# Performance work log

Hardware: AMD Instinct MI355X
Metric: run time of the kernel (lower is better)

Reference implementation:

```python
import jax, jax.numpy as jnp
import numpy as np

N, C_IN, C_OUT, NS, SP = 100000, 64, 64, 16, 8
MID = C_OUT
EPS = 1e-5


def _bn(t, g, b):
    # BatchNorm1d training-mode stats over (n, k) per channel (biased var, as torch)
    m = t.mean(axis=(0, 1))
    v = t.var(axis=(0, 1))
    return g * (t - m) / jnp.sqrt(v + EPS) + b


def setup_inputs() -> dict:
    key = jax.random.key(0)
    ks = jax.random.split(key, 24)
    s = 0.05
    d = {
        'p': jax.random.normal(ks[0], (N, 3), jnp.float32),
        'x': jax.random.normal(ks[1], (N, C_IN), jnp.float32),
        'knn_idx': jax.random.randint(ks[2], (N, NS), 0, N, jnp.int64),
        # channelMixMLPs01: Linear(3+in, ns) + Bilinear(ns, ns, ns)
        'w1': jax.random.normal(ks[3], (NS, 3 + C_IN), jnp.float32) * s,
        'b1': jnp.zeros((NS,), jnp.float32),
        'bw': jax.random.normal(ks[4], (NS, NS, NS), jnp.float32) * s,
        'bb': jnp.zeros((NS,), jnp.float32),
        # linear_p: Linear(3,3) -> BN(3) -> ReLU -> Linear(3,out)
        'lp_w1': jax.random.normal(ks[5], (3, 3), jnp.float32) * s,
        'lp_b1': jnp.zeros((3,), jnp.float32),
        'bnp_g': jnp.ones((3,), jnp.float32),
        'bnp_b': jnp.zeros((3,), jnp.float32),
        'lp_w2': jax.random.normal(ks[6], (C_OUT, 3), jnp.float32) * s,
        'lp_b2': jnp.zeros((C_OUT,), jnp.float32),
        'c1_w': jax.random.normal(ks[7], (MID, 2 * NS), jnp.float32) * s,
        'bn1_g': jnp.ones((MID,), jnp.float32),
        'bn1_b': jnp.zeros((MID,), jnp.float32),
        'c2_w': jax.random.normal(ks[8], (MID // SP, MID), jnp.float32) * s,
        'bn2_g': jnp.ones((MID // SP,), jnp.float32),
        'bn2_b': jnp.zeros((MID // SP,), jnp.float32),
        'c3_w': jax.random.normal(ks[9], (C_OUT // SP, MID // SP), jnp.float32) * s,
        'c3_b': jnp.zeros((C_OUT // SP,), jnp.float32),
        # channelMixMLPs03: Linear(in, out)
        'w3': jax.random.normal(ks[10], (C_OUT, C_IN), jnp.float32) * s,
        'b3': jnp.zeros((C_OUT,), jnp.float32),
    }
    return d


def reference(p, x, knn_idx, w1, b1, bw, bb, lp_w1, lp_b1, bnp_g, bnp_b,
              lp_w2, lp_b2, c1_w, bn1_g, bn1_b, c2_w, bn2_g, bn2_b,
              c3_w, c3_b, w3, b3):
    n = p.shape[0]
    # queryandgroup (use_xyz=True): gather neighbors, relative coords + feats
    p_r = p[knn_idx] - p[:, None, :]                 # [n, k, 3]
    x_knn = jnp.concatenate([p_r, x[knn_idx]], -1)   # [n, k, 3+c_in]
    # channelMixMLPs01: Linear -> ReLU -> Bilinear(e, e)
    e = jax.nn.relu(x_knn @ w1.T + b1)               # [n, k, ns]
    e = jnp.einsum('nki,oij,nkj->nko', e, bw, e) + bb
    # linear_p on relative coords
    pe = p_r @ lp_w1.T + lp_b1                       # [n, k, 3]
    pe = jax.nn.relu(_bn(pe, bnp_g, bnp_b))
    p_embed = pe @ lp_w2.T + lp_b2                   # [n, k, out]
    # shrink_p: n k (a b) -> sum over a -> [n, k, ns]
    p_shrink = p_embed.reshape(n, NS, C_OUT // NS, NS).sum(axis=2)
    energy = jnp.concatenate([e, p_shrink], -1)
    # channelMixMLPs02 (1x1 convs == per-point linears over channel dim)
    h = jax.nn.relu(_bn(energy @ c1_w.T, bn1_g, bn1_b))
    h = jax.nn.relu(_bn(h @ c2_w.T, bn2_g, bn2_b))
    w = jax.nn.softmax(h @ c3_w.T + c3_b, axis=1)    # [n, k, out/sp]
    # value path: Linear then gather by knn_idx
    x_v = (x @ w3.T + b3)[knn_idx]                   # [n, k, out]
    xk = (x_v + p_embed).reshape(n, NS, SP, C_OUT // SP)
    xk = (xk * w[:, :, None, :]).reshape(n, NS, C_OUT)
    x_out = xk.sum(axis=1)                           # [n, out]
    return (x_out, xk, knn_idx, p_r)
```

## Files before the change

kernel.cpp:

```cpp
#include <hip/hip_runtime.h>
#include <math.h>

#define NPTS 100000
#define KNB  16
#define NK   1600000

#define OUT_XK   6400000
#define OUT_KNN  108800000
#define OUT_PR   110400000

#define WS_BNP_RAW 0
#define WS_BN1_RAW 6
#define WS_BN2_RAW 134
#define WS_BNP_SS  160
#define WS_WS2     166
#define WS_WSB     214
#define WS_BN1_SS  230
#define WS_BN2_SS  358
#define WS_SYM     384
#define WS_C1F     2560
#define WS_C2T     2816
#define WS_E       4096
#define WS_T2      25604096
#define WS_XROW    38404096
#define WS_X1      44804096

#define GRID_NK 3125
#define NK_STRIDE 800000


__global__ __launch_bounds__(256) void k_pre(
    const float* __restrict__ x, const float* __restrict__ w3,
    const float* __restrict__ b3, const float* __restrict__ w1,
    const float* __restrict__ b1, float* __restrict__ ws)
{
    int n = blockIdx.x * 256 + threadIdx.x;
    if (n >= NPTS) return;
    float xr[64];
    const float4* xp = (const float4*)(x + (size_t)n * 64);
    #pragma unroll
    for (int i = 0; i < 16; ++i) {
        float4 v = xp[i];
        xr[4*i] = v.x; xr[4*i+1] = v.y; xr[4*i+2] = v.z; xr[4*i+3] = v.w;
    }
    float* xrow = ws + WS_XROW;
    for (int c = 0; c < 64; ++c) {
        const float* wr = w3 + c * 64;
        float a0 = b3[c], a1 = 0.f;
        #pragma unroll
        for (int q = 0; q < 64; q += 2) { a0 += wr[q] * xr[q]; a1 += wr[q+1] * xr[q+1]; }
        xrow[(size_t)n * 64 + c] = a0 + a1;
    }
    float* X1 = ws + WS_X1;
    for (int j = 0; j < 16; ++j) {
        const float* wr = w1 + j * 67 + 3;
        float a0 = b1[j], a1 = 0.f;
        #pragma unroll
        for (int q = 0; q < 64; q += 2) { a0 += wr[q] * xr[q]; a1 += wr[q+1] * xr[q+1]; }
        X1[n * 16 + j] = a0 + a1;
    }
}

__global__ void k_sym(const float* __restrict__ bw, float* __restrict__ ws)
{
    int t = blockIdx.x * 256 + threadIdx.x;
    if (t >= 136 * 16) return;
    int pair = t >> 4, o = t & 15;
    int i = 0, r = pair;
    while (r >= 16 - i) { r -= 16 - i; ++i; }
    int j = i + r;
    float v = bw[o * 256 + i * 16 + j];
    if (i != j) v += bw[o * 256 + j * 16 + i];
    ws[WS_SYM + pair * 16 + o] = v;
}

__global__ __launch_bounds__(256) void k_stage0(
    const float* __restrict__ p, const int* __restrict__ knn,
    const float* __restrict__ w1, const float* __restrict__ bb,
    const float* __restrict__ lpw1, const float* __restrict__ lpb1,
    const float* __restrict__ wsro, float* __restrict__ ws, float* __restrict__ out)
{
    __shared__ float wsym[136 * 16];
    __shared__ float e1s[2][16][256];
    __shared__ float sb[6];
    const float* symw = wsro + WS_SYM;
    const float* X1   = wsro + WS_X1;
    float* e_out = ws + WS_E;
    float* o_knn = out + OUT_KNN;
    float* o_pr  = out + OUT_PR;
    int tid = threadIdx.x;
    if (tid < 6) sb[tid] = 0.f;
    for (int k = tid; k < 136 * 16; k += 256) wsym[k] = symw[k];

    int gid = blockIdx.x * 256 + tid;
    int id0 = gid * 2;
    int n = id0 >> 4;
    float px = p[n*3+0], py = p[n*3+1], pz = p[n*3+2];
    float ps0=0.f, ps1=0.f, ps2=0.f, pq0=0.f, pq1=0.f, pq2=0.f;

    #pragma unroll
    for (int e = 0; e < 2; ++e) {
        int id = id0 + e;
        int idx = knn[id];
        float pr0 = p[idx*3+0] - px;
        float pr1 = p[idx*3+1] - py;
        float pr2 = p[idx*3+2] - pz;
        o_pr[id*3+0] = pr0; o_pr[id*3+1] = pr1; o_pr[id*3+2] = pr2;
        o_knn[id] = (float)idx;
        float v0 = lpb1[0] + lpw1[0]*pr0 + lpw1[1]*pr1 + lpw1[2]*pr2;
        float v1 = lpb1[1] + lpw1[3]*pr0 + lpw1[4]*pr1 + lpw1[5]*pr2;
        float v2 = lpb1[2] + lpw1[6]*pr0 + lpw1[7]*pr1 + lpw1[8]*pr2;
        ps0 += v0; ps1 += v1; ps2 += v2;
        pq0 += v0*v0; pq1 += v1*v1; pq2 += v2*v2;
        const float4* xg = (const float4*)(X1 + (size_t)idx * 16);
        #pragma unroll
        for (int h = 0; h < 4; ++h) {
            float4 v = xg[h];
            const float* wr = w1 + (4*h) * 67;
            e1s[e][4*h+0][tid] = fmaxf(v.x + wr[0]*pr0 + wr[1]*pr1 + wr[2]*pr2, 0.f);
            wr += 67;
            e1s[e][4*h+1][tid] = fmaxf(v.y + wr[0]*pr0 + wr[1]*pr1 + wr[2]*pr2, 0.f);
            wr += 67;
            e1s[e][4*h+2][tid] = fmaxf(v.z + wr[0]*pr0 + wr[1]*pr1 + wr[2]*pr2, 0.f);
            wr += 67;
            e1s[e][4*h+3][tid] = fmaxf(v.w + wr[0]*pr0 + wr[1]*pr1 + wr[2]*pr2, 0.f);
        }
    }
    __syncthreads();

    float acc_a[16], acc_b[16];
    #pragma unroll
    for (int o = 0; o < 16; ++o) { float bo = bb[o]; acc_a[o] = bo; acc_b[o] = bo; }

    int pair = 0;
    #pragma unroll 1
    for (int i = 0; i < 16; ++i) {
        float eai = e1s[0][i][tid];
        float ebi = e1s[1][i][tid];
        #pragma unroll 1
        for (int j = i; j < 16; ++j, ++pair) {
            float eaj = e1s[0][j][tid];
            float ebj = e1s[1][j][tid];
            float ma = eai * eaj, mb = ebi * ebj;
            const float4* wp = (const float4*)(wsym + pair * 16);
            float4 w0v = wp[0], w1v = wp[1], w2v = wp[2], w3v = wp[3];
            acc_a[0]  += w0v.x*ma; acc_a[1]  += w0v.y*ma; acc_a[2]  += w0v.z*ma; acc_a[3]  += w0v.w*ma;
            acc_a[4]  += w1v.x*ma; acc_a[5]  += w1v.y*ma; acc_a[6]  += w1v.z*ma; acc_a[7]  += w1v.w*ma;
            acc_a[8]  += w2v.x*ma; acc_a[9]  += w2v.y*ma; acc_a[10] += w2v.z*ma; acc_a[11] += w2v.w*ma;
            acc_a[12] += w3v.x*ma; acc_a[13] += w3v.y*ma; acc_a[14] += w3v.z*ma; acc_a[15] += w3v.w*ma;
            acc_b[0]  += w0v.x*mb; acc_b[1]  += w0v.y*mb; acc_b[2]  += w0v.z*mb; acc_b[3]  += w0v.w*mb;
            acc_b[4]  += w1v.x*mb; acc_b[5]  += w1v.y*mb; acc_b[6]  += w1v.z*mb; acc_b[7]  += w1v.w*mb;
            acc_b[8]  += w2v.x*mb; acc_b[9]  += w2v.y*mb; acc_b[10] += w2v.z*mb; acc_b[11] += w2v.w*mb;
            acc_b[12] += w3v.x*mb; acc_b[13] += w3v.y*mb; acc_b[14] += w3v.z*mb; acc_b[15] += w3v.w*mb;
        }
    }
    float4* eo = (float4*)(e_out + (size_t)id0 * 16);
    eo[0] = make_float4(acc_a[0],  acc_a[1],  acc_a[2],  acc_a[3]);
    eo[1] = make_float4(acc_a[4],  acc_a[5],  acc_a[6],  acc_a[7]);
    eo[2] = make_float4(acc_a[8],  acc_a[9],  acc_a[10], acc_a[11]);
    eo[3] = make_float4(acc_a[12], acc_a[13], acc_a[14], acc_a[15]);
    eo[4] = make_float4(acc_b[0],  acc_b[1],  acc_b[2],  acc_b[3]);
    eo[5] = make_float4(acc_b[4],  acc_b[5],  acc_b[6],  acc_b[7]);
    eo[6] = make_float4(acc_b[8],  acc_b[9],  acc_b[10], acc_b[11]);
    eo[7] = make_float4(acc_b[12], acc_b[13], acc_b[14], acc_b[15]);

    #pragma unroll
    for (int off = 32; off; off >>= 1) {
        ps0 += __shfl_xor(ps0, off); ps1 += __shfl_xor(ps1, off); ps2 += __shfl_xor(ps2, off);
        pq0 += __shfl_xor(pq0, off); pq1 += __shfl_xor(pq1, off); pq2 += __shfl_xor(pq2, off);
    }
    if ((tid & 63) == 0) {
        atomicAdd(&sb[0], ps0); atomicAdd(&sb[1], ps1); atomicAdd(&sb[2], ps2);
        atomicAdd(&sb[3], pq0); atomicAdd(&sb[4], pq1); atomicAdd(&sb[5], pq2);
    }
    __syncthreads();
    if (tid < 6) atomicAdd(&ws[WS_BNP_RAW + tid], sb[tid]);
}

__global__ void k_fin_bnp(float* __restrict__ ws,
    const float* __restrict__ g, const float* __restrict__ b,
    const float* __restrict__ lpw2, const float* __restrict__ lpb2)
{
    int t = threadIdx.x;
    if (t < 3) {
        float mean = ws[WS_BNP_RAW + t] / (float)NK;
        float var  = ws[WS_BNP_RAW + 3 + t] / (float)NK - mean * mean;
        float sc = g[t] * rsqrtf(var + 1e-5f);
        ws[WS_BNP_SS + t] = sc;
        ws[WS_BNP_SS + 3 + t] = b[t] - mean * sc;
    }
    if (t >= 16 && t < 64) {
        int r = t - 16, j = r / 3, d = r % 3;
        ws[WS_WS2 + r] = lpw2[(j)*3+d] + lpw2[(16+j)*3+d] + lpw2[(32+j)*3+d] + lpw2[(48+j)*3+d];
    }
    if (t >= 64 && t < 80) {
        int j = t - 64;
        ws[WS_WSB + j] = lpb2[j] + lpb2[16+j] + lpb2[32+j] + lpb2[48+j];
    }
}

__global__ void k_fold(const float* __restrict__ c1w, const float* __restrict__ c2w,
                       float* __restrict__ ws)
{
    int c = threadIdx.x;
    if (c >= 64) return;
    const float* B = c1w + c * 32 + 16;
    float m0 = 0.f, m1 = 0.f, m2 = 0.f, dd = 0.f;
    #pragma unroll
    for (int j = 0; j < 16; ++j) {
        float bj = B[j];
        m0 += bj * ws[WS_WS2 + j*3 + 0];
        m1 += bj * ws[WS_WS2 + j*3 + 1];
        m2 += bj * ws[WS_WS2 + j*3 + 2];
        dd += bj * ws[WS_WSB + j];
    }
    ws[WS_C1F + c*4 + 0] = m0;
    ws[WS_C1F + c*4 + 1] = m1;
    ws[WS_C1F + c*4 + 2] = m2;
    ws[WS_C1F + c*4 + 3] = dd;
    #pragma unroll
    for (int k = 0; k < 8; ++k)
        ws[WS_C2T + c*8 + k] = c2w[k * 64 + c];
}

__device__ __forceinline__ void build_eq(
    const float* __restrict__ e_in, const float* __restrict__ o_pr,
    const float* __restrict__ lpw1, const float* __restrict__ lpb1,
    const float* __restrict__ wsro, int id, float* e, float* q)
{
    const float4* ep = (const float4*)(e_in + (size_t)id * 16);
    #pragma unroll
    for (int i = 0; i < 4; ++i) {
        float4 v = ep[i];
        e[4*i] = v.x; e[4*i+1] = v.y; e[4*i+2] = v.z; e[4*i+3] = v.w;
    }
    float pr0 = o_pr[id*3+0], pr1 = o_pr[id*3+1], pr2 = o_pr[id*3+2];
    float v0 = lpb1[0] + lpw1[0]*pr0 + lpw1[1]*pr1 + lpw1[2]*pr2;
    float v1 = lpb1[1] + lpw1[3]*pr0 + lpw1[4]*pr1 + lpw1[5]*pr2;
    float v2 = lpb1[2] + lpw1[6]*pr0 + lpw1[7]*pr1 + lpw1[8]*pr2;
    q[0] = fmaxf(v0*wsro[WS_BNP_SS+0] + wsro[WS_BNP_SS+3], 0.f);
    q[1] = fmaxf(v1*wsro[WS_BNP_SS+1] + wsro[WS_BNP_SS+4], 0.f);
    q[2] = fmaxf(v2*wsro[WS_BNP_SS+2] + wsro[WS_BNP_SS+5], 0.f);
}

__global__ __launch_bounds__(256) void k_stats1(
    const float* __restrict__ wsro, const float* __restrict__ out_ro,
    const float* __restrict__ lpw1, const float* __restrict__ lpb1,
    const float* __restrict__ c1w, float* __restrict__ ws)
{
    __shared__ float sacc[128];
    if (threadIdx.x < 128) sacc[threadIdx.x] = 0.f;
    __syncthreads();
    const float* e_in = wsro + WS_E;
    const float* o_pr = out_ro + OUT_PR;
    int id0 = blockIdx.x * 256 + threadIdx.x;
    int id1 = id0 + NK_STRIDE;
    float e0[16], e1[16], q0[3], q1[3];
    build_eq(e_in, o_pr, lpw1, lpb1, wsro, id0, e0, q0);
    build_eq(e_in, o_pr, lpw1, lpb1, wsro, id1, e1, q1);
    #pragma unroll 1
    for (int c = 0; c < 64; c += 2) {
        const float* wa = c1w + c * 32;
        const float* wb = wa + 32;
        const float4 fa = *(const float4*)(wsro + WS_C1F + c*4);
        const float4 fb = *(const float4*)(wsro + WS_C1F + c*4 + 4);
        float hA0 = fa.w + fa.x*q0[0] + fa.y*q0[1] + fa.z*q0[2];
        float hB0 = fb.w + fb.x*q0[0] + fb.y*q0[1] + fb.z*q0[2];
        float hA1 = fa.w + fa.x*q1[0] + fa.y*q1[1] + fa.z*q1[2];
        float hB1 = fb.w + fb.x*q1[0] + fb.y*q1[1] + fb.z*q1[2];
        #pragma unroll
        for (int k = 0; k < 16; ++k) {
            hA0 += wa[k]*e0[k]; hB0 += wb[k]*e0[k];
            hA1 += wa[k]*e1[k]; hB1 += wb[k]*e1[k];
        }
        float sA = hA0 + hA1, qA = hA0*hA0 + hA1*hA1;
        float sB = hB0 + hB1, qB = hB0*hB0 + hB1*hB1;
        #pragma unroll
        for (int off = 32; off; off >>= 1) {
            sA += __shfl_xor(sA, off); qA += __shfl_xor(qA, off);
            sB += __shfl_xor(sB, off); qB += __shfl_xor(qB, off);
        }
        if ((threadIdx.x & 63) == 0) {
            atomicAdd(&sacc[c], sA);   atomicAdd(&sacc[64+c], qA);
            atomicAdd(&sacc[c+1], sB); atomicAdd(&sacc[65+c], qB);
        }
    }
    __syncthreads();
    if (threadIdx.x < 128) atomicAdd(&ws[WS_BN1_RAW + threadIdx.x], sacc[threadIdx.x]);
}

__global__ void k_fin_bn1(float* __restrict__ ws, const float* __restrict__ g, const float* __restrict__ b)
{
    int c = threadIdx.x;
    if (c < 64) {
        float mean = ws[WS_BN1_RAW + c] / (float)NK;
        float var  = ws[WS_BN1_RAW + 64 + c] / (float)NK - mean * mean;
        float sc = g[c] * rsqrtf(var + 1e-5f);
        ws[WS_BN1_SS + c] = sc;
        ws[WS_BN1_SS + 64 + c] = b[c] - mean * sc;
    }
}

__global__ __launch_bounds__(256) void k_stage2(
    const float* __restrict__ wsro, const float* __restrict__ out_ro,
    const float* __restrict__ lpw1, const float* __restrict__ lpb1,
    const float* __restrict__ c1w, float* __restrict__ ws)
{
    float tsum[8] = {0,0,0,0,0,0,0,0}, tssq[8] = {0,0,0,0,0,0,0,0};
    const float* e_in = wsro + WS_E;
    const float* o_pr = out_ro + OUT_PR;
    float* t2 = ws + WS_T2;
    int id = blockIdx.x * 256 + threadIdx.x;
    #pragma unroll 1
    for (int it = 0; it < 2; ++it, id += NK_STRIDE) {
        float e[16], q[3];
        build_eq(e_in, o_pr, lpw1, lpb1, wsro, id, e, q);
        float t2a[8] = {0,0,0,0,0,0,0,0};
        #pragma unroll 1
        for (int c = 0; c < 64; c += 2) {
            const float* wa = c1w + c * 32;
            const float* wb = wa + 32;
            const float4 fa = *(const float4*)(wsro + WS_C1F + c*4);
            const float4 fb = *(const float4*)(wsro + WS_C1F + c*4 + 4);
            float h0 = fa.w + fa.x*q[0] + fa.y*q[1] + fa.z*q[2];
            float h1 = fb.w + fb.x*q[0] + fb.y*q[1] + fb.z*q[2];
            #pragma unroll
            for (int k = 0; k < 16; ++k) {
                h0 += wa[k]*e[k]; h1 += wb[k]*e[k];
            }
            h0 = fmaxf(h0 * wsro[WS_BN1_SS + c]     + wsro[WS_BN1_SS + 64 + c], 0.f);
            h1 = fmaxf(h1 * wsro[WS_BN1_SS + c + 1] + wsro[WS_BN1_SS + 65 + c], 0.f);
            const float4 ca0 = *(const float4*)(wsro + WS_C2T + c*8);
            const float4 ca1 = *(const float4*)(wsro + WS_C2T + c*8 + 4);
            const float4 cb0 = *(const float4*)(wsro + WS_C2T + c*8 + 8);
            const float4 cb1 = *(const float4*)(wsro + WS_C2T + c*8 + 12);
            t2a[0] += h0*ca0.x + h1*cb0.x; t2a[1] += h0*ca0.y + h1*cb0.y;
            t2a[2] += h0*ca0.z + h1*cb0.z; t2a[3] += h0*ca0.w + h1*cb0.w;
            t2a[4] += h0*ca1.x + h1*cb1.x; t2a[5] += h0*ca1.y + h1*cb1.y;
            t2a[6] += h0*ca1.z + h1*cb1.z; t2a[7] += h0*ca1.w + h1*cb1.w;
        }
        float4* t2p = (float4*)(t2 + (size_t)id * 8);
        t2p[0] = make_float4(t2a[0], t2a[1], t2a[2], t2a[3]);
        t2p[1] = make_float4(t2a[4], t2a[5], t2a[6], t2a[7]);
        #pragma unroll
        for (int c2 = 0; c2 < 8; ++c2) { tsum[c2] += t2a[c2]; tssq[c2] += t2a[c2] * t2a[c2]; }
    }
    __shared__ float sacc[16];
    if (threadIdx.x < 16) sacc[threadIdx.x] = 0.f;
    __syncthreads();
    #pragma unroll
    for (int c2 = 0; c2 < 8; ++c2) {
        float s = tsum[c2], s2 = tssq[c2];
        #pragma unroll
        for (int off = 32; off; off >>= 1) { s += __shfl_xor(s, off); s2 += __shfl_xor(s2, off); }
        if ((threadIdx.x & 63) == 0) { atomicAdd(&sacc[c2], s); atomicAdd(&sacc[8 + c2], s2); }
    }
    __syncthreads();
    if (threadIdx.x < 16) atomicAdd(&ws[WS_BN2_RAW + threadIdx.x], sacc[threadIdx.x]);
}

__global__ void k_fin_bn2(float* __restrict__ ws, const float* __restrict__ g, const float* __restrict__ b)
{
    int c = threadIdx.x;
    if (c < 8) {
        float mean = ws[WS_BN2_RAW + c] / (float)NK;
        float var  = ws[WS_BN2_RAW + 8 + c] / (float)NK - mean * mean;
        float sc = g[c] * rsqrtf(var + 1e-5f);
        ws[WS_BN2_SS + c] = sc;
        ws[WS_BN2_SS + 8 + c] = b[c] - mean * sc;
    }
}

__global__ __launch_bounds__(128) void k_final(
    const int* __restrict__ knn, const float* __restrict__ wsro,
    const float* __restrict__ c3w, const float* __restrict__ c3b,
    const float* __restrict__ lpw1, const float* __restrict__ lpb1,
    const float* __restrict__ lpw2, const float* __restrict__ lpb2,
    float* __restrict__ out)
{
    int n = blockIdx.x, t = threadIdx.x;
    __shared__ float h2s[16][8], ssm[16][8], wls[16][8], pes[16][3], prs[48], red[128];
    __shared__ int idxs[16];
    const float* t2   = wsro + WS_T2;
    const float* o_pr = out + OUT_PR;
    const float* xrow = wsro + WS_XROW;
    if (t < 16) idxs[t] = knn[n * 16 + t];
    if (t < 48) prs[t] = o_pr[(size_t)n * 48 + t];
    {
        int k = t >> 3, c2 = t & 7;
        float v = t2[(size_t)n * 128 + t];
        h2s[k][c2] = fmaxf(v * wsro[WS_BN2_SS + c2] + wsro[WS_BN2_SS + 8 + c2], 0.f);
    }
    __syncthreads();
    if (t < 48) {
        int k = t / 3, d = t % 3;
        float pe = lpb1[d] + lpw1[d*3+0]*prs[k*3+0] + lpw1[d*3+1]*prs[k*3+1] + lpw1[d*3+2]*prs[k*3+2];
        pes[k][d] = fmaxf(pe * wsro[WS_BNP_SS + d] + wsro[WS_BNP_SS + 3 + d], 0.f);
    }
    {
        int k = t >> 3, cc = t & 7;
        float s = c3b[cc];
        #pragma unroll
        for (int q = 0; q < 8; ++q) s += h2s[k][q] * c3w[cc * 8 + q];
        ssm[k][cc] = s;
    }
    __syncthreads();
    if (t < 8) {
        float m = -1e30f;
        for (int k = 0; k < 16; ++k) m = fmaxf(m, ssm[k][t]);
        float sum = 0.f;
        for (int k = 0; k < 16; ++k) { float ev = __expf(ssm[k][t] - m); wls[k][t] = ev; sum += ev; }
        float inv = 1.f / sum;
        for (int k = 0; k < 16; ++k) wls[k][t] *= inv;
    }
    __syncthreads();
    int c = t & 63, kh = t >> 6;
    float w20 = lpw2[c*3], w21 = lpw2[c*3+1], w22 = lpw2[c*3+2], bc = lpb2[c];
    float acc = 0.f;
    float* out_xk = out + OUT_XK + (size_t)n * 1024;
    #pragma unroll
    for (int i = 0; i < 8; ++i) {
        int k = kh * 8 + i;
        float xv = xrow[(size_t)idxs[k] * 64 + c];
        float pemb = bc + w20 * pes[k][0] + w21 * pes[k][1] + w22 * pes[k][2];
        float val = (xv + pemb) * wls[k][c & 7];
        out_xk[k * 64 + c] = val;
        acc += val;
    }
    red[t] = acc;
    __syncthreads();
    if (t < 64) out[(size_t)n * 64 + t] = red[t] + red[t + 64];
}

extern "C" void kernel_launch(void* const* d_in, const int* in_sizes, int n_in,
                              void* d_out, int out_size, void* d_ws, size_t ws_size,
                              hipStream_t stream)
{
    (void)in_sizes; (void)n_in; (void)out_size; (void)ws_size;
    const float* p    = (const float*)d_in[0];
    const float* x    = (const float*)d_in[1];
    const int*   knn  = (const int*)  d_in[2];
    const float* w1   = (const float*)d_in[3];
    const float* b1   = (const float*)d_in[4];
    const float* bw   = (const float*)d_in[5];
    const float* bb   = (const float*)d_in[6];
    const float* lpw1 = (const float*)d_in[7];
    const float* lpb1 = (const float*)d_in[8];
    const float* bnpg = (const float*)d_in[9];
    const float* bnpb = (const float*)d_in[10];
    const float* lpw2 = (const float*)d_in[11];
    const float* lpb2 = (const float*)d_in[12];
    const float* c1w  = (const float*)d_in[13];
    const float* bn1g = (const float*)d_in[14];
    const float* bn1b = (const float*)d_in[15];
    const float* c2w  = (const float*)d_in[16];
    const float* bn2g = (const float*)d_in[17];
    const float* bn2b = (const float*)d_in[18];
    const float* c3w  = (const float*)d_in[19];
    const float* c3b  = (const float*)d_in[20];
    const float* w3   = (const float*)d_in[21];
    const float* b3   = (const float*)d_in[22];
    float* out = (float*)d_out;
    float* ws  = (float*)d_ws;

    (void)hipMemsetAsync(ws, 0, 160 * sizeof(float), stream);
    k_pre   <<<(NPTS + 255) / 256, 256, 0, stream>>>(x, w3, b3, w1, b1, ws);
    k_sym   <<<9, 256, 0, stream>>>(bw, ws);
    k_stage0<<<GRID_NK, 256, 0, stream>>>(p, knn, w1, bb, lpw1, lpb1, ws, ws, out);
    k_fin_bnp<<<1, 128, 0, stream>>>(ws, bnpg, bnpb, lpw2, lpb2);
    k_fold  <<<1, 64, 0, stream>>>(c1w, c2w, ws);
    k_stats1<<<GRID_NK, 256, 0, stream>>>(ws, out, lpw1, lpb1, c1w, ws);
    k_fin_bn1<<<1, 64, 0, stream>>>(ws, bn1g, bn1b);
    k_stage2<<<GRID_NK, 256, 0, stream>>>(ws, out, lpw1, lpb1, c1w, ws);
    k_fin_bn2<<<1, 64, 0, stream>>>(ws, bn2g, bn2b);
    k_final <<<NPTS, 128, 0, stream>>>(knn, ws, c3w, c3b, lpw1, lpb1, lpw2, lpb2, out);
}
```

Before: 709.9 us.

## Replace shuffle reductions with slotted LDS atomics and pack two points per final block

In k_stats1, the per-channel wavefront shuffle reductions are replaced by per-thread LDS atomics into a 128x66 shared array. Threads are spread over 64 slots with a per-wave offset to reduce contention, and each of the first 128 threads then sums one row. This removes the 6-step shuffle chain for each of the 32 channel pairs, but adds LDS atomic traffic and a much larger shared allocation (~33KB), which can lower occupancy. Separately, k_final processes two points per 256-thread block, halving the block count and the per-block launch overhead.

```diff
diff --git a/kernel.cpp b/kernel.cpp
--- a/kernel.cpp
+++ b/kernel.cpp
@@ -248,16 +248,18 @@
     const float* __restrict__ lpw1, const float* __restrict__ lpb1,
     const float* __restrict__ c1w, float* __restrict__ ws)
 {
-    __shared__ float sacc[128];
-    if (threadIdx.x < 128) sacc[threadIdx.x] = 0.f;
+    __shared__ float sacc[128][66];
+    int tid = threadIdx.x;
+    for (int k = tid; k < 128 * 66; k += 256) ((float*)sacc)[k] = 0.f;
     __syncthreads();
     const float* e_in = wsro + WS_E;
     const float* o_pr = out_ro + OUT_PR;
-    int id0 = blockIdx.x * 256 + threadIdx.x;
+    int id0 = blockIdx.x * 256 + tid;
     int id1 = id0 + NK_STRIDE;
     float e0[16], e1[16], q0[3], q1[3];
     build_eq(e_in, o_pr, lpw1, lpb1, wsro, id0, e0, q0);
     build_eq(e_in, o_pr, lpw1, lpb1, wsro, id1, e1, q1);
+    int slot = ((tid & 63) + 17 * (tid >> 6)) & 63;
     #pragma unroll 1
     for (int c = 0; c < 64; c += 2) {
         const float* wa = c1w + c * 32;
@@ -273,20 +275,18 @@
             hA0 += wa[k]*e0[k]; hB0 += wb[k]*e0[k];
             hA1 += wa[k]*e1[k]; hB1 += wb[k]*e1[k];
         }
-        float sA = hA0 + hA1, qA = hA0*hA0 + hA1*hA1;
-        float sB = hB0 + hB1, qB = hB0*hB0 + hB1*hB1;
-        #pragma unroll
-        for (int off = 32; off; off >>= 1) {
-            sA += __shfl_xor(sA, off); qA += __shfl_xor(qA, off);
-            sB += __shfl_xor(sB, off); qB += __shfl_xor(qB, off);
-        }
-        if ((threadIdx.x & 63) == 0) {
-            atomicAdd(&sacc[c], sA);   atomicAdd(&sacc[64+c], qA);
-            atomicAdd(&sacc[c+1], sB); atomicAdd(&sacc[65+c], qB);
-        }
-    }
-    __syncthreads();
-    if (threadIdx.x < 128) atomicAdd(&ws[WS_BN1_RAW + threadIdx.x], sacc[threadIdx.x]);
+        atomicAdd(&sacc[c][slot],      hA0 + hA1);
+        atomicAdd(&sacc[64 + c][slot], hA0*hA0 + hA1*hA1);
+        atomicAdd(&sacc[c + 1][slot],  hB0 + hB1);
+        atomicAdd(&sacc[65 + c][slot], hB0*hB0 + hB1*hB1);
+    }
+    __syncthreads();
+    if (tid < 128) {
+        float s = 0.f;
+        #pragma unroll
+        for (int i = 0; i < 64; ++i) s += sacc[tid][i];
+        atomicAdd(&ws[WS_BN1_RAW + tid], s);
+    }
 }
 
 __global__ void k_fin_bn1(float* __restrict__ ws, const float* __restrict__ g, const float* __restrict__ b)
@@ -371,65 +371,67 @@
     }
 }
 
-__global__ __launch_bounds__(128) void k_final(
+__global__ __launch_bounds__(256) void k_final(
     const int* __restrict__ knn, const float* __restrict__ wsro,
     const float* __restrict__ c3w, const float* __restrict__ c3b,
     const float* __restrict__ lpw1, const float* __restrict__ lpb1,
     const float* __restrict__ lpw2, const float* __restrict__ lpb2,
     float* __restrict__ out)
 {
-    int n = blockIdx.x, t = threadIdx.x;
-    __shared__ float h2s[16][8], ssm[16][8], wls[16][8], pes[16][3], prs[48], red[128];
-    __shared__ int idxs[16];
+    int t = threadIdx.x;
+    int sub = t >> 7, tl = t & 127;
+    int n = blockIdx.x * 2 + sub;
+    __shared__ float h2s[2][16][8], ssm[2][16][8], wls[2][16][8], pes[2][16][3], prs[2][48], red[2][128];
+    __shared__ int idxs[2][16];
     const float* t2   = wsro + WS_T2;
     const float* o_pr = out + OUT_PR;
     const float* xrow = wsro + WS_XROW;
-    if (t < 16) idxs[t] = knn[n * 16 + t];
-    if (t < 48) prs[t] = o_pr[(size_t)n * 48 + t];
+    if (tl < 16) idxs[sub][tl] = knn[n * 16 + tl];
+    if (tl < 48) prs[sub][tl] = o_pr[(size_t)n * 48 + tl];
     {
-        int k = t >> 3, c2 = t & 7;
-        float v = t2[(size_t)n * 128 + t];
-        h2s[k][c2] = fmaxf(v * wsro[WS_BN2_SS + c2] + wsro[WS_BN2_SS + 8 + c2], 0.f);
-    }
-    __syncthreads();
-    if (t < 48) {
-        int k = t / 3, d = t % 3;
-        float pe = lpb1[d] + lpw1[d*3+0]*prs[k*3+0] + lpw1[d*3+1]*prs[k*3+1] + lpw1[d*3+2]*prs[k*3+2];
-        pes[k][d] = fmaxf(pe * wsro[WS_BNP_SS + d] + wsro[WS_BNP_SS + 3 + d], 0.f);
+        int k = tl >> 3, c2 = tl & 7;
+        float v = t2[(size_t)n * 128 + tl];
+        h2s[sub][k][c2] = fmaxf(v * wsro[WS_BN2_SS + c2] + wsro[WS_BN2_SS + 8 + c2], 0.f);
+    }
+    __syncthreads();
+    if (tl < 48) {
+        int k = tl / 3, d = tl % 3;
+        float pe = lpb1[d] + lpw1[d*3+0]*prs[sub][k*3+0] + lpw1[d*3+1]*prs[sub][k*3+1] + lpw1[d*3+2]*prs[sub][k*3+2];
+        pes[sub][k][d] = fmaxf(pe * wsro[WS_BNP_SS + d] + wsro[WS_BNP_SS + 3 + d], 0.f);
     }
     {
-        int k = t >> 3, cc = t & 7;
+        int k = tl >> 3, cc = tl & 7;
         float s = c3b[cc];
         #pragma unroll
-        for (int q = 0; q < 8; ++q) s += h2s[k][q] * c3w[cc * 8 + q];
-        ssm[k][cc] = s;
-    }
-    __syncthreads();
-    if (t < 8) {
+        for (int q = 0; q < 8; ++q) s += h2s[sub][k][q] * c3w[cc * 8 + q];
+        ssm[sub][k][cc] = s;
+    }
+    __syncthreads();
+    if (tl < 8) {
         float m = -1e30f;
-        for (int k = 0; k < 16; ++k) m = fmaxf(m, ssm[k][t]);
+        for (int k = 0; k < 16; ++k) m = fmaxf(m, ssm[sub][k][tl]);
         float sum = 0.f;
-        for (int k = 0; k < 16; ++k) { float ev = __expf(ssm[k][t] - m); wls[k][t] = ev; sum += ev; }
+        for (int k = 0; k < 16; ++k) { float ev = __expf(ssm[sub][k][tl] - m); wls[sub][k][tl] = ev; sum += ev; }
         float inv = 1.f / sum;
-        for (int k = 0; k < 16; ++k) wls[k][t] *= inv;
-    }
-    __syncthreads();
-    int c = t & 63, kh = t >> 6;
+        for (int k = 0; k < 16; ++k) wls[sub][k][tl] *= inv;
+    }
+    __syncthreads();
+    int c = tl & 63, kh = tl >> 6;
     float w20 = lpw2[c*3], w21 = lpw2[c*3+1], w22 = lpw2[c*3+2], bc = lpb2[c];
     float acc = 0.f;
     float* out_xk = out + OUT_XK + (size_t)n * 1024;
     #pragma unroll
     for (int i = 0; i < 8; ++i) {
         int k = kh * 8 + i;
-        float xv = xrow[(size_t)idxs[k] * 64 + c];
-        float pemb = bc + w20 * pes[k][0] + w21 * pes[k][1] + w22 * pes[k][2];
-        float val = (xv + pemb) * wls[k][c & 7];
+        float xv = xrow[(size_t)idxs[sub][k] * 64 + c];
+        float pemb = bc + w20 * pes[sub][k][0] + w21 * pes[sub][k][1] + w22 * pes[sub][k][2];
+        float val = (xv + pemb) * wls[sub][k][c & 7];
         out_xk[k * 64 + c] = val;
         acc += val;
     }
-    red[t] = acc;
-    __syncthreads();
-    if (t < 64) out[(size_t)n * 64 + t] = red[t] + red[t + 64];
+    red[sub][tl] = acc;
+    __syncthreads();
+    if (tl < 64) out[(size_t)n * 64 + tl] = red[sub][tl] + red[sub][tl + 64];
 }
 
 extern "C" void kernel_launch(void* const* d_in, const int* in_sizes, int n_in,
@@ -473,5 +475,5 @@
     k_fin_bn1<<<1, 64, 0, stream>>>(ws, bn1g, bn1b);
     k_stage2<<<GRID_NK, 256, 0, stream>>>(ws, out, lpw1, lpb1, c1w, ws);
     k_fin_bn2<<<1, 64, 0, stream>>>(ws, bn2g, bn2b);
-    k_final <<<NPTS, 128, 0, stream>>>(knn, ws, c3w, c3b, lpw1, lpb1, lpw2, lpb2, out);
-}
+    k_final <<<NPTS / 2, 256, 0, stream>>>(knn, ws, c3w, c3b, lpw1, lpb1, lpw2, lpb2, out);
+}
```

After: 1.073 ms. 1.51x slower.
